# Kernel tuning notes

Hardware: AMD Instinct MI355X
Metric: run time of the kernel (lower is better)

The kernel has to match this reference:

```python
import jax, jax.numpy as jnp
import numpy as np

D_MODEL, NHEAD, INT_DIM = 1024, 16, 4096
HEAD_DIM = D_MODEL // NHEAD
EPS = 1e-5


def _layernorm(x, gamma, beta):
    mu = jnp.mean(x, axis=-1, keepdims=True)
    var = jnp.var(x, axis=-1, keepdims=True)
    return (x - mu) * jax.lax.rsqrt(var + EPS) * gamma + beta


def setup_inputs() -> dict:
    key = jax.random.key(0)
    ks = jax.random.split(key, 16)
    B, T = 2, 2048
    s = 0.02
    inp = {
        'x': jax.random.normal(ks[0], (B, T, D_MODEL), dtype=jnp.float32),
        'Wq': jax.random.normal(ks[1], (D_MODEL, D_MODEL), dtype=jnp.float32) * s,
        'bq': jnp.zeros((D_MODEL,), jnp.float32),
        'Wk': jax.random.normal(ks[2], (D_MODEL, D_MODEL), dtype=jnp.float32) * s,
        'bk': jnp.zeros((D_MODEL,), jnp.float32),
        'Wv': jax.random.normal(ks[3], (D_MODEL, D_MODEL), dtype=jnp.float32) * s,
        'bv': jnp.zeros((D_MODEL,), jnp.float32),
        'Wo': jax.random.normal(ks[4], (D_MODEL, D_MODEL), dtype=jnp.float32) * s,
        'bo': jnp.zeros((D_MODEL,), jnp.float32),
        'ln1_g': jnp.ones((D_MODEL,), jnp.float32),
        'ln1_b': jnp.zeros((D_MODEL,), jnp.float32),
        'ln2_g': jnp.ones((D_MODEL,), jnp.float32),
        'ln2_b': jnp.zeros((D_MODEL,), jnp.float32),
        'W1': jax.random.normal(ks[5], (D_MODEL, INT_DIM), dtype=jnp.float32) * s,
        'b1': jnp.zeros((INT_DIM,), jnp.float32),
        'W2': jax.random.normal(ks[6], (INT_DIM, D_MODEL), dtype=jnp.float32) * s,
        'b2': jnp.zeros((D_MODEL,), jnp.float32),
    }
    return inp


def reference(x, Wq, bq, Wk, bk, Wv, bv, Wo, bo, ln1_g, ln1_b, ln2_g, ln2_b, W1, b1, W2, b2):
    B, T, D = x.shape
    # projections
    q = (x @ Wq + bq).reshape(B, T, NHEAD, HEAD_DIM).transpose(0, 2, 1, 3)
    k = (x @ Wk + bk).reshape(B, T, NHEAD, HEAD_DIM).transpose(0, 2, 1, 3)
    v = (x @ Wv + bv).reshape(B, T, NHEAD, HEAD_DIM).transpose(0, 2, 1, 3)
    # attention: [B,H,T,T] scores, softmax over keys
    scores = jnp.einsum('bhqd,bhkd->bhqk', q, k) / jnp.sqrt(jnp.float32(HEAD_DIM))
    attn = jax.nn.softmax(scores, axis=-1)
    out = jnp.einsum('bhqk,bhkd->bhqd', attn, v)
    out = out.transpose(0, 2, 1, 3).reshape(B, T, D)
    attn_output = out @ Wo + bo
    # residual + layernorm 1
    h = _layernorm(x + attn_output, ln1_g, ln1_b)
    # FFN
    ff = jax.nn.relu(h @ W1 + b1) @ W2 + b2
    # residual + layernorm 2
    return _layernorm(h + ff, ln2_g, ln2_b)
```

## Files before the change

### kernel.cpp

```cpp
#include <hip/hip_runtime.h>
#include <cstdint>

#define DEVI __device__ __forceinline__

typedef float f32x4 __attribute__((ext_vector_type(4)));
typedef __bf16 bf16x8 __attribute__((ext_vector_type(8)));
typedef unsigned int u32x4v __attribute__((ext_vector_type(4)));
typedef unsigned short u16;
typedef unsigned int u32;
typedef unsigned long long u64;

#define LOG2E 1.44269504088896f
#define QSCALE (0.125f * LOG2E)

DEVI u16 bf16bits(float f) {
    u32 u = __builtin_bit_cast(u32, f);
    u32 r = u + 0x7fffu + ((u >> 16) & 1u);
    return (u16)(r >> 16);
}

DEVI float bf2f(u16 v) {
    u32 u = (u32)v << 16;
    return __builtin_bit_cast(float, u);
}

DEVI u32 pack2bf(float a, float b) {
    u16 x = __builtin_bit_cast(u16, (__bf16)a);
    u16 y = __builtin_bit_cast(u16, (__bf16)b);
    return (u32)x | ((u32)y << 16);
}

DEVI float ex2(float x) {
    float r;
    asm("v_exp_f32 %0, %1" : "=v"(r) : "v"(x));
    return r;
}

DEVI void gload16(const void* g, const void* l) {
    __builtin_amdgcn_global_load_lds(
        (const __attribute__((address_space(1))) void*)(u64)(uintptr_t)g,
        (__attribute__((address_space(3))) void*)(u32)(uintptr_t)l,
        16, 0, 0);
}

__global__ __launch_bounds__(256)
void prep_kernel(const float* __restrict__ x, u16* __restrict__ xb,
                 const float* __restrict__ Wq, const float* __restrict__ Wk,
                 const float* __restrict__ Wv, const float* __restrict__ Wo,
                 u16* __restrict__ Wqt, u16* __restrict__ Wkt,
                 u16* __restrict__ Wvt, u16* __restrict__ Wot,
                 const float* __restrict__ W1, u16* __restrict__ W1t,
                 const float* __restrict__ W2, u16* __restrict__ W2t) {
    __shared__ float t[64][65];
    const int b = blockIdx.x;
    const int tid = threadIdx.x;
    if (b < 4096) {
        int i = b * 256 + tid;
        float4 v = ((const float4*)x)[i];
        ((uint2*)xb)[i] = make_uint2(pack2bf(v.x, v.y), pack2bf(v.z, v.w));
        return;
    }
    const float* src;
    u16* dst;
    int K_, N_, k0, n0;
    if (b < 5120) {
        int l = b - 4096;
        int z = l >> 8;
        l &= 255;
        src = z == 0 ? Wq : z == 1 ? Wk : z == 2 ? Wv : Wo;
        dst = z == 0 ? Wqt : z == 1 ? Wkt : z == 2 ? Wvt : Wot;
        K_ = 1024; N_ = 1024;
        k0 = (l & 15) * 64; n0 = (l >> 4) * 64;
    } else if (b < 6144) {
        int l = b - 5120;
        src = W1; dst = W1t; K_ = 1024; N_ = 4096;
        k0 = (l & 15) * 64; n0 = (l >> 4) * 64;
    } else {
        int l = b - 6144;
        src = W2; dst = W2t; K_ = 4096; N_ = 1024;
        k0 = (l & 63) * 64; n0 = (l >> 6) * 64;
    }
#pragma unroll
    for (int i = 0; i < 16; i++) {
        int idx = i * 256 + tid;
        int r = idx >> 6, c = idx & 63;
        t[r][c] = src[(u64)(k0 + r) * N_ + n0 + c];
    }
    __syncthreads();
#pragma unroll
    for (int i = 0; i < 4; i++) {
        int idx = i * 256 + tid;
        int cq = idx & 15;
        int r = idx >> 4;
        u32 lo = (u32)bf16bits(t[cq * 4 + 0][r]) | ((u32)bf16bits(t[cq * 4 + 1][r]) << 16);
        u32 hi = (u32)bf16bits(t[cq * 4 + 2][r]) | ((u32)bf16bits(t[cq * 4 + 3][r]) << 16);
        *(uint2*)(dst + (u64)(n0 + r) * K_ + k0 + cq * 4) = make_uint2(lo, hi);
    }
}

enum { MODE_QK = 0, MODE_VT = 1, MODE_RELU = 3 };

DEVI void gemm_core(const u16* __restrict__ A, const u16* __restrict__ Bt, int K_,
                    u16 (*ldsA)[128 * 64], u16 (*ldsB)[128 * 64],
                    f32x4 (&acc)[4][4], int m0, int n0) {
    const int tid = threadIdx.x;
    const int lane = tid & 63;
    const int wid = tid >> 6;
    const int wr = wid >> 1, wc = wid & 1;
    const int l15 = lane & 15, l4 = lane >> 4;
    const int srow = tid >> 3;
    const int sc = (tid & 7) ^ (srow & 7);

    const u16* ap[4];
    const u16* bp[4];
#pragma unroll
    for (int i = 0; i < 4; i++) {
        ap[i] = A + (u64)(m0 + i * 32 + srow) * K_ + sc * 8;
        bp[i] = Bt + (u64)(n0 + i * 32 + srow) * K_ + sc * 8;
    }

    auto stageA = [&](int buf) {
#pragma unroll
        for (int i = 0; i < 4; i++) {
            gload16(ap[i], (const char*)ldsA[buf] + (i * 256 + tid) * 16);
            ap[i] += 64;
        }
    };
    auto stageB = [&](int buf) {
#pragma unroll
        for (int i = 0; i < 4; i++) {
            gload16(bp[i], (const char*)ldsB[buf] + (i * 256 + tid) * 16);
            bp[i] += 64;
        }
    };

    auto compute = [&](const u16* A_, const u16* B_) {
#pragma unroll
        for (int ks = 0; ks < 2; ks++) {
            bf16x8 af[4], bfr[4];
#pragma unroll
            for (int mi = 0; mi < 4; mi++) {
                int row = wr * 64 + mi * 16 + l15;
                af[mi] = *(const bf16x8*)((const char*)A_ + row * 128 +
                                          (((ks * 4 + l4) ^ (row & 7)) * 16));
            }
#pragma unroll
            for (int ni = 0; ni < 4; ni++) {
                int row = wc * 64 + ni * 16 + l15;
                bfr[ni] = *(const bf16x8*)((const char*)B_ + row * 128 +
                                           (((ks * 4 + l4) ^ (row & 7)) * 16));
            }
            __builtin_amdgcn_s_setprio(1);
#pragma unroll
            for (int mi = 0; mi < 4; mi++)
#pragma unroll
                for (int ni = 0; ni < 4; ni++)
                    acc[mi][ni] = __builtin_amdgcn_mfma_f32_16x16x32_bf16(
                        af[mi], bfr[ni], acc[mi][ni], 0, 0, 0);
            __builtin_amdgcn_s_setprio(0);
        }
    };

    const int nk = K_ >> 6;
    stageA(0);
    stageB(0);
    stageA(1);
    int ca = 0, cbb = 0, sa = 2, sb = 1;
    for (int t = 0; t < nk; t++) {
        if (t < nk - 1) {
            asm volatile("s_waitcnt vmcnt(4)" ::: "memory");
        } else {
            asm volatile("s_waitcnt vmcnt(0)" ::: "memory");
        }
        __builtin_amdgcn_s_barrier();
        if (t + 1 < nk) { stageB(sb); sb ^= 1; }
        if (t + 2 < nk) { stageA(sa); sa = (sa == 2) ? 0 : sa + 1; }
        compute(ldsA[ca], ldsB[cbb]);
        ca = (ca == 2) ? 0 : ca + 1;
        cbb ^= 1;
    }
}

template <int MODE>
DEVI void gemm_epilogue(f32x4 (&acc)[4][4], const float* __restrict__ bias,
                        void* __restrict__ outp, int N_, int m0, int n0,
                        float scale, u16* l16) {
    const int tid = threadIdx.x;
    const int lane = tid & 63;
    const int wid = tid >> 6;
    const int wr = wid >> 1, wc = wid & 1;
    const int l15 = lane & 15, l4 = lane >> 4;
    __syncthreads();
#pragma unroll
    for (int mi = 0; mi < 4; mi++) {
#pragma unroll
        for (int ni = 0; ni < 4; ni++) {
            const int nl = wc * 64 + ni * 16 + l15;
            const int mlb = wr * 64 + mi * 16 + l4 * 4;
            const float bv = bias[n0 + nl];
            if (MODE == MODE_VT) {
                u32 lo = pack2bf(acc[mi][ni][0] + bv, acc[mi][ni][1] + bv);
                u32 hi = pack2bf(acc[mi][ni][2] + bv, acc[mi][ni][3] + bv);
                *(uint2*)(l16 + nl * 136 + mlb) = make_uint2(lo, hi);
            } else {
#pragma unroll
                for (int r = 0; r < 4; r++) {
                    float v = acc[mi][ni][r] + bv;
                    if (MODE == MODE_RELU) v = fmaxf(v, 0.f);
                    else v = v * scale;
                    l16[(mlb + r) * 136 + nl] = bf16bits(v);
                }
            }
        }
    }
    __syncthreads();
#pragma unroll
    for (int it = 0; it < 8; it++) {
        int c = it * 256 + tid;
        int rr = c >> 4, nc = c & 15;
        u32x4v v = *(const u32x4v*)(l16 + rr * 136 + nc * 8);
        if (MODE == MODE_QK) {
            int m = m0 + rr;
            int b = m >> 11, t = m & 2047;
            int hh = (n0 >> 6) + (nc >> 3);
            int d = (nc & 7) * 8;
            *(u32x4v*)((u16*)outp + (((u64)((b << 4) + hh) * 2048 + t) << 6) + d) = v;
        } else if (MODE == MODE_VT) {
            int hh = (n0 + rr) >> 6;
            int d = (n0 + rr) & 63;
            int b = m0 >> 11, tb = m0 & 2047;
            *(u32x4v*)((u16*)outp + ((u64)((b << 4) + hh) * 64 + d) * 2048 + tb + nc * 8) = v;
        } else {
            *(u32x4v*)((u16*)outp + (u64)(m0 + rr) * N_ + n0 + nc * 8) = v;
        }
    }
}

template <int MODE>
__global__ __launch_bounds__(256, 2)
void gemm_kernel(const u16* __restrict__ A, const u16* __restrict__ Bt,
                 const float* __restrict__ bias, void* __restrict__ outp,
                 int N_, int K_) {
    __shared__ u16 ldsA[3][128 * 64];
    __shared__ u16 ldsB[2][128 * 64];
    const int m0 = blockIdx.x * 128;
    const int n0 = blockIdx.y * 128;
    f32x4 acc[4][4];
#pragma unroll
    for (int i = 0; i < 4; i++)
#pragma unroll
        for (int j = 0; j < 4; j++) acc[i][j] = (f32x4){0.f, 0.f, 0.f, 0.f};
    gemm_core(A, Bt, K_, ldsA, ldsB, acc, m0, n0);
    gemm_epilogue<MODE>(acc, bias, outp, N_, m0, n0, 1.f, (u16*)ldsA);
}

__global__ __launch_bounds__(256, 2)
void gemm_qkv_kernel(const u16* __restrict__ A,
                     const u16* __restrict__ Wq, const u16* __restrict__ Wk,
                     const u16* __restrict__ Wv,
                     const float* __restrict__ bq, const float* __restrict__ bk,
                     const float* __restrict__ bv,
                     u16* __restrict__ Qo, u16* __restrict__ Ko, u16* __restrict__ Vo) {
    __shared__ u16 ldsA[3][128 * 64];
    __shared__ u16 ldsB[2][128 * 64];
    const int z = blockIdx.z;
    const u16* Bt = z == 0 ? Wq : z == 1 ? Wk : Wv;
    const float* bias = z == 0 ? bq : z == 1 ? bk : bv;
    const int m0 = blockIdx.x * 128;
    const int n0 = blockIdx.y * 128;
    f32x4 acc[4][4];
#pragma unroll
    for (int i = 0; i < 4; i++)
#pragma unroll
        for (int j = 0; j < 4; j++) acc[i][j] = (f32x4){0.f, 0.f, 0.f, 0.f};
    gemm_core(A, Bt, 1024, ldsA, ldsB, acc, m0, n0);
    if (z == 2)
        gemm_epilogue<MODE_VT>(acc, bias, Vo, 1024, m0, n0, 1.f, (u16*)ldsA);
    else
        gemm_epilogue<MODE_QK>(acc, bias, z == 0 ? Qo : Ko, 1024, m0, n0,
                               z == 0 ? QSCALE : 1.f, (u16*)ldsA);
}

template <bool RB16>
__global__ __launch_bounds__(256, 2)
void gemm64_kernel(const u16* __restrict__ A, const u16* __restrict__ Bt,
                   const float* __restrict__ bias, const void* __restrict__ resid,
                   float* __restrict__ outp, int K_) {
    __shared__ u16 ldsA[3][128 * 64];
    __shared__ u16 ldsB[3][64 * 64];
    const int tid = threadIdx.x;
    const int lane = tid & 63;
    const int wid = tid >> 6;
    const int m0 = blockIdx.x * 128;
    const int n0 = blockIdx.y * 64;
    const int l15 = lane & 15, l4 = lane >> 4;
    const int srow = tid >> 3;
    const int sc = (tid & 7) ^ (srow & 7);

    const u16* ap[4];
    const u16* bp[2];
#pragma unroll
    for (int i = 0; i < 4; i++)
        ap[i] = A + (u64)(m0 + i * 32 + srow) * K_ + sc * 8;
#pragma unroll
    for (int i = 0; i < 2; i++)
        bp[i] = Bt + (u64)(n0 + i * 32 + srow) * K_ + sc * 8;

    auto stage = [&](int buf) {
#pragma unroll
        for (int i = 0; i < 4; i++) {
            gload16(ap[i], (const char*)ldsA[buf] + (i * 256 + tid) * 16);
            ap[i] += 64;
        }
#pragma unroll
        for (int i = 0; i < 2; i++) {
            gload16(bp[i], (const char*)ldsB[buf] + (i * 256 + tid) * 16);
            bp[i] += 64;
        }
    };

    f32x4 acc[2][4];
#pragma unroll
    for (int i = 0; i < 2; i++)
#pragma unroll
        for (int j = 0; j < 4; j++) acc[i][j] = (f32x4){0.f, 0.f, 0.f, 0.f};

    auto compute = [&](const u16* A_, const u16* B_) {
#pragma unroll
        for (int ks = 0; ks < 2; ks++) {
            bf16x8 af[2], bfr[4];
#pragma unroll
            for (int mi = 0; mi < 2; mi++) {
                int row = wid * 32 + mi * 16 + l15;
                af[mi] = *(const bf16x8*)((const char*)A_ + row * 128 +
                                          (((ks * 4 + l4) ^ (row & 7)) * 16));
            }
#pragma unroll
            for (int ni = 0; ni < 4; ni++) {
                int row = ni * 16 + l15;
                bfr[ni] = *(const bf16x8*)((const char*)B_ + row * 128 +
                                           (((ks * 4 + l4) ^ (row & 7)) * 16));
            }
            __builtin_amdgcn_s_setprio(1);
#pragma unroll
            for (int mi = 0; mi < 2; mi++)
#pragma unroll
                for (int ni = 0; ni < 4; ni++)
                    acc[mi][ni] = __builtin_amdgcn_mfma_f32_16x16x32_bf16(
                        af[mi], bfr[ni], acc[mi][ni], 0, 0, 0);
            __builtin_amdgcn_s_setprio(0);
        }
    };

    const int nk = K_ >> 6;
    stage(0);
    stage(1);
    int cb = 0, sb = 2;
    for (int t = 0; t < nk; t++) {
        if (t < nk - 1) {
            asm volatile("s_waitcnt vmcnt(6)" ::: "memory");
        } else {
            asm volatile("s_waitcnt vmcnt(0)" ::: "memory");
        }
        __builtin_amdgcn_s_barrier();
        if (t + 2 < nk) stage(sb);
        compute(ldsA[cb], ldsB[cb]);
        cb = (cb == 2) ? 0 : cb + 1;
        sb = (sb == 2) ? 0 : sb + 1;
    }

    float* fl = (float*)ldsA;
    __syncthreads();
#pragma unroll
    for (int mi = 0; mi < 2; mi++) {
#pragma unroll
        for (int ni = 0; ni < 4; ni++) {
            const int nl = ni * 16 + l15;
            const int mlb = wid * 32 + mi * 16 + l4 * 4;
#pragma unroll
            for (int r = 0; r < 4; r++)
                fl[(mlb + r) * 68 + nl] = acc[mi][ni][r];
        }
    }
    __syncthreads();
#pragma unroll
    for (int it = 0; it < 8; it++) {
        int c = it * 256 + tid;
        int rr = c >> 4, nc = c & 15;
        f32x4 v = *(const f32x4*)(fl + rr * 68 + nc * 4);
        const int n = n0 + nc * 4;
        float4 bv = *(const float4*)(bias + n);
        const u64 i2 = (u64)(m0 + rr) * 1024 + n;
        float4 rv;
        if (RB16) {
            uint2 rb = *(const uint2*)((const u16*)resid + i2);
            rv.x = bf2f((u16)(rb.x & 0xffffu)); rv.y = bf2f((u16)(rb.x >> 16));
            rv.z = bf2f((u16)(rb.y & 0xffffu)); rv.w = bf2f((u16)(rb.y >> 16));
        } else {
            rv = *(const float4*)((const float*)resid + i2);
        }
        float4 o;
        o.x = v[0] + bv.x + rv.x;
        o.y = v[1] + bv.y + rv.y;
        o.z = v[2] + bv.z + rv.z;
        o.w = v[3] + bv.w + rv.w;
        *(float4*)(outp + i2) = o;
    }
}

__global__ __launch_bounds__(256, 3)
void attn_kernel(const u16* __restrict__ Qg, const u16* __restrict__ Kg,
                 const u16* __restrict__ Vtg, u16* __restrict__ Og) {
    __shared__ u16 ldsK[3][64 * 64];
    __shared__ u16 ldsV[3][64 * 64];
    const int tid = threadIdx.x;
    const int lane = tid & 63;
    const int w = tid >> 6;
    const int l15 = lane & 15, l4 = lane >> 4;
    const int id = blockIdx.x;
    const int swz = (id & 7) * 128 + (id >> 3);
    const int bh = swz >> 5;
    const int qblk = swz & 31;
    const u64 kvbase = (u64)bh * 2048 * 64;
    const int qw0 = qblk * 64 + w * 16;

    const int srow = tid >> 3;
    const int sc8 = ((tid & 7) ^ (srow & 7)) * 8;
    const u16* kq0 = Kg + kvbase + (u64)srow * 64 + sc8;
    const u16* kq1 = Kg + kvbase + (u64)(srow + 32) * 64 + sc8;
    const u16* vq0 = Vtg + kvbase + (u64)srow * 2048 + sc8;
    const u16* vq1 = Vtg + kvbase + (u64)(srow + 32) * 2048 + sc8;

    auto stage = [&](int buf) {
        gload16(kq0, (const char*)ldsK[buf] + tid * 16);
        gload16(kq1, (const char*)ldsK[buf] + (256 + tid) * 16);
        gload16(vq0, (const char*)ldsV[buf] + tid * 16);
        gload16(vq1, (const char*)ldsV[buf] + (256 + tid) * 16);
        kq0 += 4096; kq1 += 4096; vq0 += 64; vq1 += 64;
    };

    bf16x8 aq[2];
#pragma unroll
    for (int ks = 0; ks < 2; ks++)
        aq[ks] = *(const bf16x8*)(Qg + kvbase + (u64)(qw0 + l15) * 64 + ks * 32 + l4 * 8);
    asm volatile("s_waitcnt vmcnt(0)" ::: "memory");

    stage(0);
    stage(1);

    const u32x4v onesw = {0x3F803F80u, 0x3F803F80u, 0x3F803F80u, 0x3F803F80u};
    const bf16x8 aones = __builtin_bit_cast(bf16x8, onesw);

    f32x4 acco[4];
#pragma unroll
    for (int i = 0; i < 4; i++) acco[i] = (f32x4){0.f, 0.f, 0.f, 0.f};
    f32x4 lacc = (f32x4){0.f, 0.f, 0.f, 0.f};

    auto tile_body = [&](const u16* K_, const u16* V_) {
        f32x4 sf[4];
#pragma unroll
        for (int f = 0; f < 4; f++) sf[f] = (f32x4){0.f, 0.f, 0.f, 0.f};
#pragma unroll
        for (int ks = 0; ks < 2; ks++) {
            bf16x8 ak[4];
#pragma unroll
            for (int f = 0; f < 4; f++) {
                int row = f * 16 + l15;
                ak[f] = *(const bf16x8*)((const char*)K_ + row * 128 +
                                         (((ks * 4 + l4) ^ (row & 7)) * 16));
            }
            __builtin_amdgcn_s_setprio(1);
#pragma unroll
            for (int f = 0; f < 4; f++)
                sf[f] = __builtin_amdgcn_mfma_f32_16x16x32_bf16(ak[f], aq[ks], sf[f], 0, 0, 0);
            __builtin_amdgcn_s_setprio(0);
        }

        u32 A[4], B[4];
#pragma unroll
        for (int f = 0; f < 4; f++) {
            float p0 = ex2(sf[f][0]);
            float p1 = ex2(sf[f][1]);
            float p2 = ex2(sf[f][2]);
            float p3 = ex2(sf[f][3]);
            A[f] = pack2bf(p0, p1);
            B[f] = pack2bf(p2, p3);
        }
        asm volatile("v_permlane32_swap_b32 %0, %1" : "+v"(A[0]), "+v"(A[1]));
        asm volatile("v_permlane16_swap_b32 %0, %1" : "+v"(A[0]), "+v"(A[1]));
        asm volatile("v_permlane32_swap_b32 %0, %1" : "+v"(B[0]), "+v"(B[1]));
        asm volatile("v_permlane16_swap_b32 %0, %1" : "+v"(B[0]), "+v"(B[1]));
        asm volatile("v_permlane32_swap_b32 %0, %1" : "+v"(A[2]), "+v"(A[3]));
        asm volatile("v_permlane16_swap_b32 %0, %1" : "+v"(A[2]), "+v"(A[3]));
        asm volatile("v_permlane32_swap_b32 %0, %1" : "+v"(B[2]), "+v"(B[3]));
        asm volatile("v_permlane16_swap_b32 %0, %1" : "+v"(B[2]), "+v"(B[3]));

#pragma unroll
        for (int ks = 0; ks < 2; ks++) {
            u32x4v pw = {A[2 * ks], B[2 * ks], A[2 * ks + 1], B[2 * ks + 1]};
            bf16x8 pfrag = __builtin_bit_cast(bf16x8, pw);
            bf16x8 av[4];
#pragma unroll
            for (int nf = 0; nf < 4; nf++) {
                int row = nf * 16 + l15;
                av[nf] = *(const bf16x8*)((const char*)V_ + row * 128 +
                                          (((ks * 4 + l4) ^ (row & 7)) * 16));
            }
            __builtin_amdgcn_s_setprio(1);
            lacc = __builtin_amdgcn_mfma_f32_16x16x32_bf16(aones, pfrag, lacc, 0, 0, 0);
#pragma unroll
            for (int nf = 0; nf < 4; nf++)
                acco[nf] = __builtin_amdgcn_mfma_f32_16x16x32_bf16(av[nf], pfrag, acco[nf], 0, 0, 0);
            __builtin_amdgcn_s_setprio(0);
        }
    };

    int cb = 0;
    int sb = 2;
    for (int t = 0; t < 31; t++) {
        asm volatile("s_waitcnt vmcnt(4)" ::: "memory");
        __builtin_amdgcn_s_barrier();
        if (t < 30) stage(sb);
        tile_body(ldsK[cb], ldsV[cb]);
        cb = (cb == 2) ? 0 : cb + 1;
        sb = (sb == 2) ? 0 : sb + 1;
    }
    asm volatile("s_waitcnt vmcnt(0)" ::: "memory");
    __builtin_amdgcn_s_barrier();
    tile_body(ldsK[cb], ldsV[cb]);

    const float inv = 1.f / lacc[0];

    const int b = bh >> 4, h = bh & 15;
    const int tq = qw0 + l15;
#pragma unroll
    for (int nf = 0; nf < 4; nf++) {
        const int d = nf * 16 + l4 * 4;
        u32 lo = pack2bf(acco[nf][0] * inv, acco[nf][1] * inv);
        u32 hi = pack2bf(acco[nf][2] * inv, acco[nf][3] * inv);
        *(uint2*)(Og + ((u64)(b * 2048 + tq) << 10) + h * 64 + d) = make_uint2(lo, hi);
    }
}

template <bool WF32, bool WB16>
__global__ __launch_bounds__(256, 4)
void ln_kernel(const float* __restrict__ in, const float* __restrict__ gam,
               const float* __restrict__ bet, float* __restrict__ outf,
               u16* __restrict__ outb) {
    __shared__ float red[2][4];
    const int row = blockIdx.x;
    const int tid = threadIdx.x;
    float4 v = ((const float4*)(in + (u64)row * 1024))[tid];
    float s = v.x + v.y + v.z + v.w;
    float sq = v.x * v.x + v.y * v.y + v.z * v.z + v.w * v.w;
#pragma unroll
    for (int sh = 1; sh < 64; sh <<= 1) {
        s += __shfl_xor(s, sh, 64);
        sq += __shfl_xor(sq, sh, 64);
    }
    if ((tid & 63) == 0) { red[0][tid >> 6] = s; red[1][tid >> 6] = sq; }
    __syncthreads();
    s = red[0][0] + red[0][1] + red[0][2] + red[0][3];
    sq = red[1][0] + red[1][1] + red[1][2] + red[1][3];
    float mu = s * (1.f / 1024.f);
    float var = sq * (1.f / 1024.f) - mu * mu;
    float inv = rsqrtf(var + 1e-5f);
    float4 g = ((const float4*)gam)[tid];
    float4 bb = ((const float4*)bet)[tid];
    float4 o;
    o.x = (v.x - mu) * inv * g.x + bb.x;
    o.y = (v.y - mu) * inv * g.y + bb.y;
    o.z = (v.z - mu) * inv * g.z + bb.z;
    o.w = (v.w - mu) * inv * g.w + bb.w;
    if (WF32) ((float4*)(outf + (u64)row * 1024))[tid] = o;
    if (WB16) {
        ((uint2*)(outb + (u64)row * 1024))[tid] = make_uint2(pack2bf(o.x, o.y), pack2bf(o.z, o.w));
    }
}

extern "C" void kernel_launch(void* const* d_in, const int* in_sizes, int n_in,
                              void* d_out, int out_size, void* d_ws, size_t ws_size,
                              hipStream_t stream) {
    (void)in_sizes; (void)n_in; (void)out_size; (void)ws_size;
    const float* x  = (const float*)d_in[0];
    const float* Wq = (const float*)d_in[1];
    const float* bq = (const float*)d_in[2];
    const float* Wk = (const float*)d_in[3];
    const float* bk = (const float*)d_in[4];
    const float* Wv = (const float*)d_in[5];
    const float* bv = (const float*)d_in[6];
    const float* Wo = (const float*)d_in[7];
    const float* bo = (const float*)d_in[8];
    const float* g1 = (const float*)d_in[9];
    const float* be1 = (const float*)d_in[10];
    const float* g2 = (const float*)d_in[11];
    const float* be2 = (const float*)d_in[12];
    const float* W1 = (const float*)d_in[13];
    const float* b1 = (const float*)d_in[14];
    const float* W2 = (const float*)d_in[15];
    const float* b2 = (const float*)d_in[16];

    char* ws = (char*)d_ws;
    const u64 MB = 1024ull * 1024ull;
    u16* xb    = (u16*)(ws + 0);
    u16* Wqt   = (u16*)(ws + 8 * MB);
    u16* Wkt   = (u16*)(ws + 10 * MB);
    u16* Wvt   = (u16*)(ws + 12 * MB);
    u16* Wot   = (u16*)(ws + 14 * MB);
    u16* W1t   = (u16*)(ws + 16 * MB);
    u16* W2t   = (u16*)(ws + 24 * MB);
    u16* Qb    = (u16*)(ws + 32 * MB);
    u16* Kb    = (u16*)(ws + 40 * MB);
    u16* Vtb   = (u16*)(ws + 48 * MB);
    u16* Ob    = (u16*)(ws + 56 * MB);
    float* pre1 = (float*)(ws + 64 * MB);
    u16* hb    = (u16*)(ws + 96 * MB);
    u16* ffb   = (u16*)(ws + 104 * MB);
    float* pre2 = (float*)(ws + 80 * MB);

    prep_kernel<<<7168, 256, 0, stream>>>(x, xb, Wq, Wk, Wv, Wo,
                                          Wqt, Wkt, Wvt, Wot, W1, W1t, W2, W2t);

    gemm_qkv_kernel<<<dim3(32, 8, 3), 256, 0, stream>>>(xb, Wqt, Wkt, Wvt,
                                                        bq, bk, bv, Qb, Kb, Vtb);

    attn_kernel<<<1024, 256, 0, stream>>>(Qb, Kb, Vtb, Ob);

    gemm64_kernel<false><<<dim3(32, 16), 256, 0, stream>>>(Ob, Wot, bo, x, pre1, 1024);
    ln_kernel<false, true><<<4096, 256, 0, stream>>>(pre1, g1, be1, nullptr, hb);
    gemm_kernel<MODE_RELU><<<dim3(32, 32), 256, 0, stream>>>(hb, W1t, b1, ffb, 4096, 1024);
    gemm64_kernel<true><<<dim3(32, 16), 256, 0, stream>>>(ffb, W2t, b2, hb, pre2, 4096);
    ln_kernel<true, false><<<4096, 256, 0, stream>>>(pre2, g2, be2, (float*)d_out, nullptr);
}
```

Before: 202.4 us.

## Split GEMM tiles across eight waves and simplify to double-buffered pipeline

All GEMM kernels move from 256-thread to 512-thread blocks, with launch bounds of 4 blocks per CU. Each wave now computes half as many output fragments, which halves its accumulator registers and is meant to give more waves to hide latency. The main GEMM core also drops its triple-buffered A and staggered vmcnt waits for a plain two-buffer ping-pong that drains all loads before every barrier. That trades away load/compute overlap, and the tight register budget and per-block LDS use may cap the occupancy actually reached.

```diff
diff --git a/kernel.cpp b/kernel.cpp
--- a/kernel.cpp
+++ b/kernel.cpp
@@ -42,6 +42,10 @@
         (__attribute__((address_space(3))) void*)(u32)(uintptr_t)l,
         16, 0, 0);
 }
+
+#define VMCNT0_BARRIER()                                   \
+    asm volatile("s_waitcnt vmcnt(0)" ::: "memory");       \
+    __builtin_amdgcn_s_barrier()
 
 __global__ __launch_bounds__(256)
 void prep_kernel(const float* __restrict__ x, u16* __restrict__ xb,
@@ -102,45 +106,42 @@
 
 DEVI void gemm_core(const u16* __restrict__ A, const u16* __restrict__ Bt, int K_,
                     u16 (*ldsA)[128 * 64], u16 (*ldsB)[128 * 64],
-                    f32x4 (&acc)[4][4], int m0, int n0) {
+                    f32x4 (&acc)[2][4], int m0, int n0) {
     const int tid = threadIdx.x;
     const int lane = tid & 63;
-    const int wid = tid >> 6;
-    const int wr = wid >> 1, wc = wid & 1;
+    const int w = tid >> 6;
+    const int wr = w >> 1, wc = w & 1;
     const int l15 = lane & 15, l4 = lane >> 4;
     const int srow = tid >> 3;
     const int sc = (tid & 7) ^ (srow & 7);
 
-    const u16* ap[4];
-    const u16* bp[4];
-#pragma unroll
-    for (int i = 0; i < 4; i++) {
-        ap[i] = A + (u64)(m0 + i * 32 + srow) * K_ + sc * 8;
-        bp[i] = Bt + (u64)(n0 + i * 32 + srow) * K_ + sc * 8;
-    }
-
-    auto stageA = [&](int buf) {
-#pragma unroll
-        for (int i = 0; i < 4; i++) {
-            gload16(ap[i], (const char*)ldsA[buf] + (i * 256 + tid) * 16);
+    const u16* ap[2];
+    const u16* bp[2];
+    ap[0] = A + (u64)(m0 + srow) * K_ + sc * 8;
+    ap[1] = A + (u64)(m0 + 64 + srow) * K_ + sc * 8;
+    bp[0] = Bt + (u64)(n0 + srow) * K_ + sc * 8;
+    bp[1] = Bt + (u64)(n0 + 64 + srow) * K_ + sc * 8;
+
+    auto stage = [&](int buf) {
+#pragma unroll
+        for (int i = 0; i < 2; i++) {
+            gload16(ap[i], (const char*)ldsA[buf] + (i * 512 + tid) * 16);
             ap[i] += 64;
         }
+#pragma unroll
+        for (int i = 0; i < 2; i++) {
+            gload16(bp[i], (const char*)ldsB[buf] + (i * 512 + tid) * 16);
+            bp[i] += 64;
+        }
     };
-    auto stageB = [&](int buf) {
-#pragma unroll
-        for (int i = 0; i < 4; i++) {
-            gload16(bp[i], (const char*)ldsB[buf] + (i * 256 + tid) * 16);
-            bp[i] += 64;
-        }
-    };
 
     auto compute = [&](const u16* A_, const u16* B_) {
 #pragma unroll
         for (int ks = 0; ks < 2; ks++) {
-            bf16x8 af[4], bfr[4];
-#pragma unroll
-            for (int mi = 0; mi < 4; mi++) {
-                int row = wr * 64 + mi * 16 + l15;
+            bf16x8 af[2], bfr[4];
+#pragma unroll
+            for (int mi = 0; mi < 2; mi++) {
+                int row = wr * 32 + mi * 16 + l15;
                 af[mi] = *(const bf16x8*)((const char*)A_ + row * 128 +
                                           (((ks * 4 + l4) ^ (row & 7)) * 16));
             }
@@ -152,7 +153,7 @@
             }
             __builtin_amdgcn_s_setprio(1);
 #pragma unroll
-            for (int mi = 0; mi < 4; mi++)
+            for (int mi = 0; mi < 2; mi++)
 #pragma unroll
                 for (int ni = 0; ni < 4; ni++)
                     acc[mi][ni] = __builtin_amdgcn_mfma_f32_16x16x32_bf16(
@@ -162,41 +163,34 @@
     };
 
     const int nk = K_ >> 6;
-    stageA(0);
-    stageB(0);
-    stageA(1);
-    int ca = 0, cbb = 0, sa = 2, sb = 1;
-    for (int t = 0; t < nk; t++) {
-        if (t < nk - 1) {
-            asm volatile("s_waitcnt vmcnt(4)" ::: "memory");
-        } else {
-            asm volatile("s_waitcnt vmcnt(0)" ::: "memory");
-        }
-        __builtin_amdgcn_s_barrier();
-        if (t + 1 < nk) { stageB(sb); sb ^= 1; }
-        if (t + 2 < nk) { stageA(sa); sa = (sa == 2) ? 0 : sa + 1; }
-        compute(ldsA[ca], ldsB[cbb]);
-        ca = (ca == 2) ? 0 : ca + 1;
-        cbb ^= 1;
+    stage(0);
+    VMCNT0_BARRIER();
+    for (int t = 0; t < nk; t += 2) {
+        if (t + 1 < nk) stage(1);
+        compute(ldsA[0], ldsB[0]);
+        VMCNT0_BARRIER();
+        if (t + 2 < nk) stage(0);
+        compute(ldsA[1], ldsB[1]);
+        VMCNT0_BARRIER();
     }
 }
 
 template <int MODE>
-DEVI void gemm_epilogue(f32x4 (&acc)[4][4], const float* __restrict__ bias,
+DEVI void gemm_epilogue(f32x4 (&acc)[2][4], const float* __restrict__ bias,
                         void* __restrict__ outp, int N_, int m0, int n0,
                         float scale, u16* l16) {
     const int tid = threadIdx.x;
     const int lane = tid & 63;
-    const int wid = tid >> 6;
-    const int wr = wid >> 1, wc = wid & 1;
+    const int w = tid >> 6;
+    const int wr = w >> 1, wc = w & 1;
     const int l15 = lane & 15, l4 = lane >> 4;
     __syncthreads();
 #pragma unroll
-    for (int mi = 0; mi < 4; mi++) {
+    for (int mi = 0; mi < 2; mi++) {
 #pragma unroll
         for (int ni = 0; ni < 4; ni++) {
             const int nl = wc * 64 + ni * 16 + l15;
-            const int mlb = wr * 64 + mi * 16 + l4 * 4;
+            const int mlb = wr * 32 + mi * 16 + l4 * 4;
             const float bv = bias[n0 + nl];
             if (MODE == MODE_VT) {
                 u32 lo = pack2bf(acc[mi][ni][0] + bv, acc[mi][ni][1] + bv);
@@ -215,8 +209,8 @@
     }
     __syncthreads();
 #pragma unroll
-    for (int it = 0; it < 8; it++) {
-        int c = it * 256 + tid;
+    for (int it = 0; it < 4; it++) {
+        int c = it * 512 + tid;
         int rr = c >> 4, nc = c & 15;
         u32x4v v = *(const u32x4v*)(l16 + rr * 136 + nc * 8);
         if (MODE == MODE_QK) {
@@ -237,40 +231,40 @@
 }
 
 template <int MODE>
-__global__ __launch_bounds__(256, 2)
+__global__ __launch_bounds__(512, 4)
 void gemm_kernel(const u16* __restrict__ A, const u16* __restrict__ Bt,
                  const float* __restrict__ bias, void* __restrict__ outp,
                  int N_, int K_) {
-    __shared__ u16 ldsA[3][128 * 64];
+    __shared__ u16 ldsA[2][128 * 64];
     __shared__ u16 ldsB[2][128 * 64];
     const int m0 = blockIdx.x * 128;
     const int n0 = blockIdx.y * 128;
-    f32x4 acc[4][4];
-#pragma unroll
-    for (int i = 0; i < 4; i++)
+    f32x4 acc[2][4];
+#pragma unroll
+    for (int i = 0; i < 2; i++)
 #pragma unroll
         for (int j = 0; j < 4; j++) acc[i][j] = (f32x4){0.f, 0.f, 0.f, 0.f};
     gemm_core(A, Bt, K_, ldsA, ldsB, acc, m0, n0);
     gemm_epilogue<MODE>(acc, bias, outp, N_, m0, n0, 1.f, (u16*)ldsA);
 }
 
-__global__ __launch_bounds__(256, 2)
+__global__ __launch_bounds__(512, 4)
 void gemm_qkv_kernel(const u16* __restrict__ A,
                      const u16* __restrict__ Wq, const u16* __restrict__ Wk,
                      const u16* __restrict__ Wv,
                      const float* __restrict__ bq, const float* __restrict__ bk,
                      const float* __restrict__ bv,
                      u16* __restrict__ Qo, u16* __restrict__ Ko, u16* __restrict__ Vo) {
-    __shared__ u16 ldsA[3][128 * 64];
+    __shared__ u16 ldsA[2][128 * 64];
     __shared__ u16 ldsB[2][128 * 64];
     const int z = blockIdx.z;
     const u16* Bt = z == 0 ? Wq : z == 1 ? Wk : Wv;
     const float* bias = z == 0 ? bq : z == 1 ? bk : bv;
     const int m0 = blockIdx.x * 128;
     const int n0 = blockIdx.y * 128;
-    f32x4 acc[4][4];
-#pragma unroll
-    for (int i = 0; i < 4; i++)
+    f32x4 acc[2][4];
+#pragma unroll
+    for (int i = 0; i < 2; i++)
 #pragma unroll
         for (int j = 0; j < 4; j++) acc[i][j] = (f32x4){0.f, 0.f, 0.f, 0.f};
     gemm_core(A, Bt, 1024, ldsA, ldsB, acc, m0, n0);
@@ -282,7 +276,7 @@
 }
 
 template <bool RB16>
-__global__ __launch_bounds__(256, 2)
+__global__ __launch_bounds__(512, 4)
 void gemm64_kernel(const u16* __restrict__ A, const u16* __restrict__ Bt,
                    const float* __restrict__ bias, const void* __restrict__ resid,
                    float* __restrict__ outp, int K_) {
@@ -290,50 +284,41 @@
     __shared__ u16 ldsB[3][64 * 64];
     const int tid = threadIdx.x;
     const int lane = tid & 63;
-    const int wid = tid >> 6;
+    const int w = tid >> 6;
+    const int l15 = lane & 15, l4 = lane >> 4;
     const int m0 = blockIdx.x * 128;
     const int n0 = blockIdx.y * 64;
-    const int l15 = lane & 15, l4 = lane >> 4;
     const int srow = tid >> 3;
     const int sc = (tid & 7) ^ (srow & 7);
 
-    const u16* ap[4];
-    const u16* bp[2];
-#pragma unroll
-    for (int i = 0; i < 4; i++)
-        ap[i] = A + (u64)(m0 + i * 32 + srow) * K_ + sc * 8;
-#pragma unroll
-    for (int i = 0; i < 2; i++)
-        bp[i] = Bt + (u64)(n0 + i * 32 + srow) * K_ + sc * 8;
+    const u16* ap[2];
+    const u16* bp0;
+    ap[0] = A + (u64)(m0 + srow) * K_ + sc * 8;
+    ap[1] = A + (u64)(m0 + 64 + srow) * K_ + sc * 8;
+    bp0 = Bt + (u64)(n0 + srow) * K_ + sc * 8;
 
     auto stage = [&](int buf) {
 #pragma unroll
-        for (int i = 0; i < 4; i++) {
-            gload16(ap[i], (const char*)ldsA[buf] + (i * 256 + tid) * 16);
+        for (int i = 0; i < 2; i++) {
+            gload16(ap[i], (const char*)ldsA[buf] + (i * 512 + tid) * 16);
             ap[i] += 64;
         }
-#pragma unroll
-        for (int i = 0; i < 2; i++) {
-            gload16(bp[i], (const char*)ldsB[buf] + (i * 256 + tid) * 16);
-            bp[i] += 64;
-        }
+        gload16(bp0, (const char*)ldsB[buf] + tid * 16);
+        bp0 += 64;
     };
 
-    f32x4 acc[2][4];
-#pragma unroll
-    for (int i = 0; i < 2; i++)
-#pragma unroll
-        for (int j = 0; j < 4; j++) acc[i][j] = (f32x4){0.f, 0.f, 0.f, 0.f};
+    f32x4 acc[4];
+#pragma unroll
+    for (int j = 0; j < 4; j++) acc[j] = (f32x4){0.f, 0.f, 0.f, 0.f};
 
     auto compute = [&](const u16* A_, const u16* B_) {
 #pragma unroll
         for (int ks = 0; ks < 2; ks++) {
-            bf16x8 af[2], bfr[4];
-#pragma unroll
-            for (int mi = 0; mi < 2; mi++) {
-                int row = wid * 32 + mi * 16 + l15;
-                af[mi] = *(const bf16x8*)((const char*)A_ + row * 128 +
-                                          (((ks * 4 + l4) ^ (row & 7)) * 16));
+            bf16x8 af, bfr[4];
+            {
+                int row = w * 16 + l15;
+                af = *(const bf16x8*)((const char*)A_ + row * 128 +
+                                      (((ks * 4 + l4) ^ (row & 7)) * 16));
             }
 #pragma unroll
             for (int ni = 0; ni < 4; ni++) {
@@ -343,11 +328,8 @@
             }
             __builtin_amdgcn_s_setprio(1);
 #pragma unroll
-            for (int mi = 0; mi < 2; mi++)
-#pragma unroll
-                for (int ni = 0; ni < 4; ni++)
-                    acc[mi][ni] = __builtin_amdgcn_mfma_f32_16x16x32_bf16(
-                        af[mi], bfr[ni], acc[mi][ni], 0, 0, 0);
+            for (int ni = 0; ni < 4; ni++)
+                acc[ni] = __builtin_amdgcn_mfma_f32_16x16x32_bf16(af, bfr[ni], acc[ni], 0, 0, 0);
             __builtin_amdgcn_s_setprio(0);
         }
     };
@@ -358,7 +340,7 @@
     int cb = 0, sb = 2;
     for (int t = 0; t < nk; t++) {
         if (t < nk - 1) {
-            asm volatile("s_waitcnt vmcnt(6)" ::: "memory");
+            asm volatile("s_waitcnt vmcnt(3)" ::: "memory");
         } else {
             asm volatile("s_waitcnt vmcnt(0)" ::: "memory");
         }
@@ -372,20 +354,17 @@
     float* fl = (float*)ldsA;
     __syncthreads();
 #pragma unroll
-    for (int mi = 0; mi < 2; mi++) {
-#pragma unroll
-        for (int ni = 0; ni < 4; ni++) {
-            const int nl = ni * 16 + l15;
-            const int mlb = wid * 32 + mi * 16 + l4 * 4;
-#pragma unroll
-            for (int r = 0; r < 4; r++)
-                fl[(mlb + r) * 68 + nl] = acc[mi][ni][r];
-        }
+    for (int ni = 0; ni < 4; ni++) {
+        const int nl = ni * 16 + l15;
+        const int mlb = w * 16 + l4 * 4;
+#pragma unroll
+        for (int r = 0; r < 4; r++)
+            fl[(mlb + r) * 68 + nl] = acc[ni][r];
     }
     __syncthreads();
 #pragma unroll
-    for (int it = 0; it < 8; it++) {
-        int c = it * 256 + tid;
+    for (int it = 0; it < 4; it++) {
+        int c = it * 512 + tid;
         int rr = c >> 4, nc = c & 15;
         f32x4 v = *(const f32x4*)(fl + rr * 68 + nc * 4);
         const int n = n0 + nc * 4;
@@ -621,14 +600,14 @@
     prep_kernel<<<7168, 256, 0, stream>>>(x, xb, Wq, Wk, Wv, Wo,
                                           Wqt, Wkt, Wvt, Wot, W1, W1t, W2, W2t);
 
-    gemm_qkv_kernel<<<dim3(32, 8, 3), 256, 0, stream>>>(xb, Wqt, Wkt, Wvt,
+    gemm_qkv_kernel<<<dim3(32, 8, 3), 512, 0, stream>>>(xb, Wqt, Wkt, Wvt,
                                                         bq, bk, bv, Qb, Kb, Vtb);
 
     attn_kernel<<<1024, 256, 0, stream>>>(Qb, Kb, Vtb, Ob);
 
-    gemm64_kernel<false><<<dim3(32, 16), 256, 0, stream>>>(Ob, Wot, bo, x, pre1, 1024);
+    gemm64_kernel<false><<<dim3(32, 16), 512, 0, stream>>>(Ob, Wot, bo, x, pre1, 1024);
     ln_kernel<false, true><<<4096, 256, 0, stream>>>(pre1, g1, be1, nullptr, hb);
-    gemm_kernel<MODE_RELU><<<dim3(32, 32), 256, 0, stream>>>(hb, W1t, b1, ffb, 4096, 1024);
-    gemm64_kernel<true><<<dim3(32, 16), 256, 0, stream>>>(ffb, W2t, b2, hb, pre2, 4096);
+    gemm_kernel<MODE_RELU><<<dim3(32, 32), 512, 0, stream>>>(hb, W1t, b1, ffb, 4096, 1024);
+    gemm64_kernel<true><<<dim3(32, 16), 512, 0, stream>>>(ffb, W2t, b2, hb, pre2, 4096);
     ln_kernel<true, false><<<4096, 256, 0, stream>>>(pre2, g2, be2, (float*)d_out, nullptr);
 }
```

Measured after the change: 202.5 us. No clear change (+0.1%).
